# Kernel optimization log

Measured on AMD Instinct MI355X. Metric: run time of the kernel, lower is better.

The kernel has to match this reference:

```python
import jax, jax.numpy as jnp
import numpy as np

EPS = 1e-5
NUM_HEADS = 6


def _dwconv_bn(x5, W, g, b, m, v, stride):
    # x5: [B, C, H, W, D]; depthwise conv3d (groups=C), kernel 3, pad 1, then eval BatchNorm3d,
    # then rearrange 'b c h w d -> b (h w d) c'
    C = x5.shape[1]
    y = jax.lax.conv_general_dilated(
        x5, W, window_strides=(stride, stride, stride), padding=[(1, 1)] * 3,
        feature_group_count=C, dimension_numbers=('NCDHW', 'OIDHW', 'NCDHW'))
    inv = g / jnp.sqrt(v + EPS)
    y = y * inv[None, :, None, None, None] + (b - m * inv)[None, :, None, None, None]
    B, C2, H, Wd, D = y.shape
    return y.transpose(0, 2, 3, 4, 1).reshape(B, H * Wd * D, C2)


def setup_inputs() -> dict:
    key = jax.random.key(0)
    ks = jax.random.split(key, 24)
    B, T, C = 8, 4096, 384
    hh = ww = dd = 16
    s = 0.02
    inp = {
        'x': jax.random.normal(ks[0], (B, T, C), jnp.float32),
        'conv_q_w': jax.random.normal(ks[1], (C, 1, 3, 3, 3), jnp.float32) * 0.1,
        'conv_k_w': jax.random.normal(ks[2], (C, 1, 3, 3, 3), jnp.float32) * 0.1,
        'conv_v_w': jax.random.normal(ks[3], (C, 1, 3, 3, 3), jnp.float32) * 0.1,
        'bn_q_g': jax.random.uniform(ks[4], (C,), jnp.float32, 0.5, 1.5),
        'bn_q_b': jax.random.normal(ks[5], (C,), jnp.float32) * 0.1,
        'bn_q_m': jax.random.normal(ks[6], (C,), jnp.float32) * 0.1,
        'bn_q_v': jax.random.uniform(ks[7], (C,), jnp.float32, 0.5, 1.5),
        'bn_k_g': jax.random.uniform(ks[8], (C,), jnp.float32, 0.5, 1.5),
        'bn_k_b': jax.random.normal(ks[9], (C,), jnp.float32) * 0.1,
        'bn_k_m': jax.random.normal(ks[10], (C,), jnp.float32) * 0.1,
        'bn_k_v': jax.random.uniform(ks[11], (C,), jnp.float32, 0.5, 1.5),
        'bn_v_g': jax.random.uniform(ks[12], (C,), jnp.float32, 0.5, 1.5),
        'bn_v_b': jax.random.normal(ks[13], (C,), jnp.float32) * 0.1,
        'bn_v_m': jax.random.normal(ks[14], (C,), jnp.float32) * 0.1,
        'bn_v_v': jax.random.uniform(ks[15], (C,), jnp.float32, 0.5, 1.5),
        'wq': jax.random.normal(ks[16], (C, C), jnp.float32) * s,
        'wk': jax.random.normal(ks[17], (C, C), jnp.float32) * s,
        'wv': jax.random.normal(ks[18], (C, C), jnp.float32) * s,
        'proj_w': jax.random.normal(ks[19], (C, C), jnp.float32) * s,
        'proj_b': jax.random.normal(ks[20], (C,), jnp.float32) * s,
        'h': hh, 'w': ww, 'd': dd,
    }
    return inp


def reference(x, conv_q_w, conv_k_w, conv_v_w,
              bn_q_g, bn_q_b, bn_q_m, bn_q_v,
              bn_k_g, bn_k_b, bn_k_m, bn_k_v,
              bn_v_g, bn_v_b, bn_v_m, bn_v_v,
              wq, wk, wv, proj_w, proj_b, h, w, d):
    B, T, C = x.shape
    H = NUM_HEADS
    Dh = C // H
    scale = C ** (-0.5)  # dim_out ** -0.5
    x5 = x.reshape(B, h, w, d, C).transpose(0, 4, 1, 2, 3)  # b (h w d) c -> b c h w d
    q = _dwconv_bn(x5, conv_q_w, bn_q_g, bn_q_b, bn_q_m, bn_q_v, 1)   # [B, T, C]
    k = _dwconv_bn(x5, conv_k_w, bn_k_g, bn_k_b, bn_k_m, bn_k_v, 2)   # [B, Tkv, C]
    v = _dwconv_bn(x5, conv_v_w, bn_v_g, bn_v_b, bn_v_m, bn_v_v, 2)   # [B, Tkv, C]

    def to_heads(t, W):  # Linear (no bias) then 'b t (h d) -> b h t d'
        z = t @ W.T
        return z.reshape(B, -1, H, Dh).transpose(0, 2, 1, 3)

    q = to_heads(q, wq)
    k = to_heads(k, wk)
    v = to_heads(v, wv)
    attn = jax.nn.softmax(jnp.einsum('bhld,bhtd->bhlt', q, k) * scale, axis=-1)
    o = jnp.einsum('bhlt,bhtd->bhld', attn, v)
    o = o.transpose(0, 2, 1, 3).reshape(B, -1, C)  # b h t d -> b t (h d)
    return o @ proj_w.T + proj_b
```

## Files before the change

kernel.cpp:

```cpp
#include <hip/hip_runtime.h>
#include <hip/hip_bf16.h>
#include <stdint.h>


typedef _Float16 f16;
typedef _Float16 f16x8 __attribute__((ext_vector_type(8)));
typedef _Float16 f16x2 __attribute__((ext_vector_type(2)));
typedef float f32x4 __attribute__((ext_vector_type(4)));
typedef float f32x16 __attribute__((ext_vector_type(16)));
typedef uint32_t u32;
typedef uint32_t u32x4 __attribute__((ext_vector_type(4)));

#define NC 384
#define MFMA16(A_,B_,C_) __builtin_amdgcn_mfma_f32_16x16x32_f16((A_),(B_),(C_),0,0,0)
#define MFMA32(A_,B_,C_) __builtin_amdgcn_mfma_f32_32x32x16_f16((A_),(B_),(C_),0,0,0)

__device__ __forceinline__ void gll16(const void* g, void* l) {
  __builtin_amdgcn_global_load_lds(
      (__attribute__((address_space(1))) void*)g,
      (__attribute__((address_space(3))) void*)l, 16, 0, 0);
}

__device__ __forceinline__ u32 pkf16(float lo, float hi) {
  return __builtin_bit_cast(u32, __builtin_amdgcn_cvt_pkrtz(lo, hi));
}

__global__ __launch_bounds__(256) void cvt_w(
    const float* __restrict__ s0, const float* __restrict__ s1,
    const float* __restrict__ s2, const float* __restrict__ s3,
    f16* __restrict__ d0, f16* __restrict__ d1,
    f16* __restrict__ d2, f16* __restrict__ d3, int n, float scq)
{
  int i = blockIdx.x * 256 + threadIdx.x;
  if (i < n) {
    d0[i] = (f16)(s0[i] * scq);
    d1[i] = (f16)s1[i]; d2[i] = (f16)s2[i]; d3[i] = (f16)s3[i];
  }
}

__global__ __launch_bounds__(384) void cvt_wt(
    const float* __restrict__ wq, const float* __restrict__ wk, const float* __restrict__ wv,
    float* __restrict__ qT, float* __restrict__ kT, float* __restrict__ vT)
{
  const int c = threadIdx.x;
  const int t = blockIdx.x;
  qT[t * 384 + c] = wq[c * 27 + t];
  kT[t * 384 + c] = wk[c * 27 + t];
  vT[t * 384 + c] = wv[c * 27 + t];
}

__global__ __launch_bounds__(128) void conv_fused(
    const float* __restrict__ x,
    const float* __restrict__ wqT, const float* __restrict__ wkT, const float* __restrict__ wvT,
    const float* __restrict__ bqg, const float* __restrict__ bqb,
    const float* __restrict__ bqm, const float* __restrict__ bqv,
    const float* __restrict__ bkg, const float* __restrict__ bkb,
    const float* __restrict__ bkm, const float* __restrict__ bkv,
    const float* __restrict__ bvg, const float* __restrict__ bvb,
    const float* __restrict__ bvm, const float* __restrict__ bvv,
    f16* __restrict__ qout, f16* __restrict__ kout, f16* __restrict__ vout)
{
  const int tile = blockIdx.x / 3, cthird = blockIdx.x % 3;
  const int c = cthird * 128 + threadIdx.x;
  const int th = tile >> 3, tw = tile & 7;
  const int b = blockIdx.y;
  const int z0 = blockIdx.z * 8;
  const int h0 = th * 2, w0 = tw * 2;

  float wqr[27], wkr[27], wvr[27];
#pragma unroll
  for (int t = 0; t < 27; ++t) {
    wqr[t] = wqT[t * 384 + c];
    wkr[t] = wkT[t * 384 + c];
    wvr[t] = wvT[t * 384 + c];
  }
  float invq = bqg[c] * rsqrtf(bqv[c] + 1e-5f), betq = bqb[c] - bqm[c] * invq;
  float invk = bkg[c] * rsqrtf(bkv[c] + 1e-5f), betk = bkb[c] - bkm[c] * invk;
  float invv = bvg[c] * rsqrtf(bvv[c] + 1e-5f), betv = bvb[c] - bvm[c] * invv;

  bool hok[4], wok[4];
#pragma unroll
  for (int a = 0; a < 4; ++a) {
    hok[a] = (unsigned)(h0 - 1 + a) < 16u;
    wok[a] = (unsigned)(w0 - 1 + a) < 16u;
  }
  const float* xb = x + (size_t)b * 4096 * NC + c;

  float win[3][4][4];
  auto ldplane = [&](int s, int iz) {
    const bool zok = (unsigned)iz < 16u;
#pragma unroll
    for (int a = 0; a < 4; ++a)
#pragma unroll
      for (int e = 0; e < 4; ++e) {
        float v = 0.f;
        if (zok && hok[a] && wok[e])
          v = xb[(size_t)((h0 - 1 + a) * 256 + (w0 - 1 + e) * 16 + iz) * NC];
        win[s][a][e] = v;
      }
  };
  ldplane(2, z0 - 1);
  ldplane(0, z0);

#pragma unroll
  for (int zr = 0; zr < 8; ++zr) {
    const int z = z0 + zr;
    const int snew = (zr + 1) % 3;
    ldplane(snew, z + 1);
    float aq00 = 0.f, aq01 = 0.f, aq10 = 0.f, aq11 = 0.f;
    float ak = 0.f, av = 0.f;
#pragma unroll
    for (int p = 0; p < 3; ++p) {
      const int s = (zr - 1 + p + 3) % 3;
#pragma unroll
      for (int a = 0; a < 3; ++a)
#pragma unroll
        for (int e = 0; e < 3; ++e) {
          const float w00 = win[s][a][e],     w01 = win[s][a][e + 1];
          const float w10 = win[s][a + 1][e], w11 = win[s][a + 1][e + 1];
          const float cq = wqr[a * 9 + e * 3 + p];
          aq00 += w00 * cq; aq01 += w01 * cq;
          aq10 += w10 * cq; aq11 += w11 * cq;
          if ((zr & 1) == 0) {
            ak += w00 * wkr[a * 9 + e * 3 + p];
            av += w00 * wvr[a * 9 + e * 3 + p];
          }
        }
    }
    const size_t qb = (size_t)b * 4096;
    qout[(qb + (h0 + 0) * 256 + (w0 + 0) * 16 + z) * NC + c] = (f16)(aq00 * invq + betq);
    qout[(qb + (h0 + 0) * 256 + (w0 + 1) * 16 + z) * NC + c] = (f16)(aq01 * invq + betq);
    qout[(qb + (h0 + 1) * 256 + (w0 + 0) * 16 + z) * NC + c] = (f16)(aq10 * invq + betq);
    qout[(qb + (h0 + 1) * 256 + (w0 + 1) * 16 + z) * NC + c] = (f16)(aq11 * invq + betq);
    if ((zr & 1) == 0) {
      const size_t t = (size_t)b * 512 + (th * 8 + tw) * 8 + (z >> 1);
      kout[t * NC + c] = (f16)(ak * invk + betk);
      vout[t * NC + c] = (f16)(av * invv + betv);
    }
  }
}

template<int MODE>
__global__ __launch_bounds__(256) void gemm_bt(
    const f16* __restrict__ A, const f16* __restrict__ Bw,
    void* __restrict__ Cout, const float* __restrict__ bias)
{
  __shared__ f16 As[128 * 64];
  __shared__ f16 Bs[128 * 64];
  const int tid = threadIdx.x;
  const int w = tid >> 6, lane = tid & 63;
  const int g = lane >> 4, q = lane & 15;
  const int wr = w >> 1, wc = w & 1;
  const size_t brow = (size_t)blockIdx.y * 128;
  const int bcol = blockIdx.x * 128;
  const int srow = lane >> 3;
  const int sbb  = (lane & 7) ^ (srow & 7);
  f32x4 acc[4][4] = {};
  for (int kt = 0; kt < 6; ++kt) {
    const int k0 = kt * 64;
#pragma unroll
    for (int j = 0; j < 4; ++j) {
      const int s = w * 4 + j;
      gll16(A  + (brow + (size_t)(s * 8 + srow)) * NC + k0 + sbb * 8, (char*)As + s * 1024);
      gll16(Bw + (size_t)(bcol + s * 8 + srow) * NC + k0 + sbb * 8, (char*)Bs + s * 1024);
    }
    __syncthreads();
#pragma unroll
    for (int ks = 0; ks < 2; ++ks) {
      f16x8 af[4], bfr[4];
      const int bb = ((g + 4 * ks) ^ (q & 7)) * 16;
#pragma unroll
      for (int m = 0; m < 4; ++m) {
        af[m]  = *(const f16x8*)((const char*)As + (wr * 64 + m * 16 + q) * 128 + bb);
        bfr[m] = *(const f16x8*)((const char*)Bs + (wc * 64 + m * 16 + q) * 128 + bb);
      }
#pragma unroll
      for (int m = 0; m < 4; ++m)
#pragma unroll
        for (int n = 0; n < 4; ++n)
          acc[m][n] = MFMA16(af[m], bfr[n], acc[m][n]);
    }
    __syncthreads();
  }
  float bvals[4];
  if (MODE == 2) {
#pragma unroll
    for (int n = 0; n < 4; ++n) bvals[n] = bias[bcol + wc * 64 + n * 16 + q];
  }
#pragma unroll
  for (int m = 0; m < 4; ++m) {
#pragma unroll
    for (int n = 0; n < 4; ++n) {
#pragma unroll
      for (int r = 0; r < 4; ++r) {
        const size_t row = brow + wr * 64 + m * 16 + 4 * g + r;
        const int col = bcol + wc * 64 + n * 16 + q;
        const float v = acc[m][n][r];
        if (MODE == 0) {
          ((f16*)Cout)[row * NC + col] = (f16)v;
        } else if (MODE == 1) {
          const size_t bi = row >> 9, t = row & 511;
          ((f16*)Cout)[(bi * NC + col) * 512 + t] = (f16)v;
        } else {
          ((float*)Cout)[row * NC + col] = v + bvals[n];
        }
      }
    }
  }
}

__global__ __launch_bounds__(256) void attn(
    const f16* __restrict__ Qp, const f16* __restrict__ Kp,
    const f16* __restrict__ Vt, f16* __restrict__ O)
{
  __shared__ f16 Ks[2][64 * 64];
  __shared__ f16 Vs[2][64 * 64];
  const int tid = threadIdx.x;
  const int w = tid >> 6, lane = tid & 63;
  const int c = lane & 31, h = lane >> 5;
  const int qt = blockIdx.x, hh = blockIdx.y, b = blockIdx.z;
  const size_t qrow = (size_t)b * 4096 + qt * 128 + w * 32 + c;

  f16x8 qf[4];
#pragma unroll
  for (int ks = 0; ks < 4; ++ks)
    qf[ks] = *(const f16x8*)(Qp + qrow * NC + hh * 64 + ks * 16 + 8 * h);

  f32x16 oa0 = {}, oa1 = {};
  float l_run = 0.f;

  const int r0 = tid >> 3, k0b = tid & 7;
  const int r1 = (tid + 256) >> 3, k1b = tid & 7;
  const f16* ks0 = Kp + ((size_t)b * 512 + r0) * NC + hh * 64 + ((k0b ^ (r0 & 7)) * 8);
  const f16* ks1 = Kp + ((size_t)b * 512 + r1) * NC + hh * 64 + ((k1b ^ (r1 & 7)) * 8);
  const f16* vs0 = Vt + ((size_t)b * NC + hh * 64 + r0) * 512 + ((k0b ^ (r0 & 7)) * 8);
  const f16* vs1 = Vt + ((size_t)b * NC + hh * 64 + r1) * 512 + ((k1b ^ (r1 & 7)) * 8);
  gll16(ks0, (char*)&Ks[0][0] + tid * 16);
  gll16(ks1, (char*)&Ks[0][0] + (tid + 256) * 16);
  gll16(vs0, (char*)&Vs[0][0] + tid * 16);
  gll16(vs1, (char*)&Vs[0][0] + (tid + 256) * 16);

  int buf = 0;
  for (int ch = 0; ch < 8; ++ch) {
    __syncthreads();
    if (ch < 7) {
      gll16(ks0 + (size_t)(ch + 1) * 64 * NC, (char*)&Ks[buf ^ 1][0] + tid * 16);
      gll16(ks1 + (size_t)(ch + 1) * 64 * NC, (char*)&Ks[buf ^ 1][0] + (tid + 256) * 16);
      gll16(vs0 + (ch + 1) * 64, (char*)&Vs[buf ^ 1][0] + tid * 16);
      gll16(vs1 + (ch + 1) * 64, (char*)&Vs[buf ^ 1][0] + (tid + 256) * 16);
    }
    const char* kb = (const char*)&Ks[buf][0];
    const char* vb = (const char*)&Vs[buf][0];
#pragma unroll
    for (int half = 0; half < 2; ++half) {
      f32x16 st = {};
#pragma unroll
      for (int ks = 0; ks < 4; ++ks) {
        const int bo = ((2 * ks + h) ^ (c & 7)) * 16;
        const f16x8 kf = *(const f16x8*)(kb + (32 * half + c) * 128 + bo);
        st = MFMA32(kf, qf[ks], st);
      }
      u32 pk[8];
      float ps0 = 0.f, ps1 = 0.f;
#pragma unroll
      for (int t = 0; t < 8; ++t) {
        const float a0 = exp2f(st[2 * t]);
        const float a1 = exp2f(st[2 * t + 1]);
        ps0 += a0; ps1 += a1;
        pk[t] = pkf16(a0, a1);
      }
      l_run += ps0 + ps1;
#pragma unroll
      for (int ss = 0; ss < 2; ++ss) {
        const int s = half * 2 + ss, tb = ss * 4;
        const u32 xs = h ? pk[tb + 0] : pk[tb + 2];
        const u32 ys = h ? pk[tb + 1] : pk[tb + 3];
        const u32 rx = __shfl_xor(xs, 32);
        const u32 ry = __shfl_xor(ys, 32);
        u32x4 fi;
        fi[0] = h ? rx : pk[tb + 0];
        fi[1] = h ? ry : pk[tb + 1];
        fi[2] = h ? pk[tb + 2] : rx;
        fi[3] = h ? pk[tb + 3] : ry;
        const f16x8 pfrag = __builtin_bit_cast(f16x8, fi);
        const int bo = ((2 * s + h) ^ (c & 7)) * 16;
        const f16x8 v0 = *(const f16x8*)(vb + c * 128 + bo);
        const f16x8 v1 = *(const f16x8*)(vb + (32 + c) * 128 + bo);
        oa0 = MFMA32(v0, pfrag, oa0);
        oa1 = MFMA32(v1, pfrag, oa1);
      }
    }
    buf ^= 1;
  }
  const float ltot = l_run + __shfl_xor(l_run, 32);
  const float linv = 1.0f / ltot;
  f16* orow = O + qrow * NC + hh * 64;
#pragma unroll
  for (int dt = 0; dt < 2; ++dt) {
#pragma unroll
    for (int qd = 0; qd < 4; ++qd) {
      const float v0 = (dt ? oa1[4 * qd + 0] : oa0[4 * qd + 0]) * linv;
      const float v1 = (dt ? oa1[4 * qd + 1] : oa0[4 * qd + 1]) * linv;
      const float v2 = (dt ? oa1[4 * qd + 2] : oa0[4 * qd + 2]) * linv;
      const float v3 = (dt ? oa1[4 * qd + 3] : oa0[4 * qd + 3]) * linv;
      uint2 pr; pr.x = pkf16(v0, v1); pr.y = pkf16(v2, v3);
      *(uint2*)(orow + dt * 32 + 8 * qd + 4 * h) = pr;
    }
  }
}

extern "C" void kernel_launch(void* const* d_in, const int* in_sizes, int n_in,
                              void* d_out, int out_size, void* d_ws, size_t ws_size,
                              hipStream_t stream) {
  const float* x   = (const float*)d_in[0];
  const float* cqw = (const float*)d_in[1];
  const float* ckw = (const float*)d_in[2];
  const float* cvw = (const float*)d_in[3];
  const float* bqg = (const float*)d_in[4],  *bqb = (const float*)d_in[5];
  const float* bqm = (const float*)d_in[6],  *bqv = (const float*)d_in[7];
  const float* bkg = (const float*)d_in[8],  *bkb = (const float*)d_in[9];
  const float* bkm = (const float*)d_in[10], *bkv = (const float*)d_in[11];
  const float* bvg = (const float*)d_in[12], *bvb = (const float*)d_in[13];
  const float* bvm = (const float*)d_in[14], *bvv = (const float*)d_in[15];
  const float* wq = (const float*)d_in[16];
  const float* wk = (const float*)d_in[17];
  const float* wv = (const float*)d_in[18];
  const float* pw = (const float*)d_in[19];
  const float* pb = (const float*)d_in[20];

  f16* q_tok = (f16*)d_out;
  f16* Qp    = (f16*)((char*)d_out + 25165824);

  char* ws = (char*)d_ws;
  f16* wq_h  = (f16*)(ws + 0);
  f16* wk_h  = (f16*)(ws + 294912);
  f16* wv_h  = (f16*)(ws + 589824);
  f16* pw_h  = (f16*)(ws + 884736);
  f16* k_tok = (f16*)(ws + 1179648);
  f16* v_tok = (f16*)(ws + 4325376);
  f16* Kp    = (f16*)(ws + 7471104);
  f16* Vt    = (f16*)(ws + 10616832);
  f16* Oi    = (f16*)(ws + 13762560);
  float* wqT = (float*)(ws + 38928384);
  float* wkT = (float*)(ws + 38969856);
  float* wvT = (float*)(ws + 39011328);

  const float scq = 0.051031036307982884f * 1.4426950408889634f;
  cvt_w<<<dim3(576), dim3(256), 0, stream>>>(wq, wk, wv, pw, wq_h, wk_h, wv_h, pw_h,
                                             147456, scq);
  cvt_wt<<<dim3(27), dim3(384), 0, stream>>>(cqw, ckw, cvw, wqT, wkT, wvT);
  conv_fused<<<dim3(192, 8, 2), dim3(128), 0, stream>>>(
      x, wqT, wkT, wvT,
      bqg, bqb, bqm, bqv, bkg, bkb, bkm, bkv, bvg, bvb, bvm, bvv,
      q_tok, k_tok, v_tok);
  gemm_bt<0><<<dim3(3, 256), dim3(256), 0, stream>>>(q_tok, wq_h, Qp, nullptr);
  gemm_bt<0><<<dim3(3, 32),  dim3(256), 0, stream>>>(k_tok, wk_h, Kp, nullptr);
  gemm_bt<1><<<dim3(3, 32),  dim3(256), 0, stream>>>(v_tok, wv_h, Vt, nullptr);
  attn<<<dim3(32, 6, 8), dim3(256), 0, stream>>>(Qp, Kp, Vt, Oi);
  gemm_bt<2><<<dim3(3, 256), dim3(256), 0, stream>>>(Oi, pw_h, d_out, pb);
}
```

Baseline: 155.6 us.

## Split fused depthwise conv into separate Q and strided K/V kernels

Replaces the single conv kernel that computed Q, K and V together with two kernels. conv_q processes 4 z-slices per block, so it launches twice as many blocks, and holds only the Q weights. conv_kv keeps just a 3x3 window per plane for the strided K/V convs. The aim is to lower register pressure, raise occupancy and parallelism, and drop the divergent even-z K/V branch. The cost is one extra launch and a second read of x, plus extra halo loads from the shorter z runs.

```diff
diff --git a/kernel.cpp b/kernel.cpp
--- a/kernel.cpp
+++ b/kernel.cpp
@@ -5,7 +5,6 @@
 
 typedef _Float16 f16;
 typedef _Float16 f16x8 __attribute__((ext_vector_type(8)));
-typedef _Float16 f16x2 __attribute__((ext_vector_type(2)));
 typedef float f32x4 __attribute__((ext_vector_type(4)));
 typedef float f32x16 __attribute__((ext_vector_type(16)));
 typedef uint32_t u32;
@@ -49,16 +48,84 @@
   vT[t * 384 + c] = wv[c * 27 + t];
 }
 
-__global__ __launch_bounds__(128) void conv_fused(
-    const float* __restrict__ x,
-    const float* __restrict__ wqT, const float* __restrict__ wkT, const float* __restrict__ wvT,
+__global__ __launch_bounds__(128) void conv_q(
+    const float* __restrict__ x, const float* __restrict__ wqT,
     const float* __restrict__ bqg, const float* __restrict__ bqb,
     const float* __restrict__ bqm, const float* __restrict__ bqv,
+    f16* __restrict__ qout)
+{
+  const int tile = blockIdx.x / 3, cthird = blockIdx.x % 3;
+  const int c = cthird * 128 + threadIdx.x;
+  const int th = tile >> 3, tw = tile & 7;
+  const int b = blockIdx.y;
+  const int z0 = blockIdx.z * 4;
+  const int h0 = th * 2, w0 = tw * 2;
+
+  float wqr[27];
+#pragma unroll
+  for (int t = 0; t < 27; ++t) wqr[t] = wqT[t * 384 + c];
+  const float invq = bqg[c] * rsqrtf(bqv[c] + 1e-5f);
+  const float betq = bqb[c] - bqm[c] * invq;
+
+  bool hok[4], wok[4];
+#pragma unroll
+  for (int a = 0; a < 4; ++a) {
+    hok[a] = (unsigned)(h0 - 1 + a) < 16u;
+    wok[a] = (unsigned)(w0 - 1 + a) < 16u;
+  }
+  const float* xb = x + (size_t)b * 4096 * NC + c;
+
+  float win[3][4][4];
+  auto ldplane = [&](int s, int iz) {
+    const bool zok = (unsigned)iz < 16u;
+#pragma unroll
+    for (int a = 0; a < 4; ++a)
+#pragma unroll
+      for (int e = 0; e < 4; ++e) {
+        float v = 0.f;
+        if (zok && hok[a] && wok[e])
+          v = xb[(size_t)((h0 - 1 + a) * 256 + (w0 - 1 + e) * 16 + iz) * NC];
+        win[s][a][e] = v;
+      }
+  };
+  ldplane(0, z0 - 1);
+  ldplane(1, z0);
+
+#pragma unroll
+  for (int zr = 0; zr < 4; ++zr) {
+    const int z = z0 + zr;
+    ldplane((zr + 2) % 3, z + 1);
+    float aq00 = 0.f, aq01 = 0.f, aq10 = 0.f, aq11 = 0.f;
+#pragma unroll
+    for (int p = 0; p < 3; ++p) {
+      const int s = (zr + p) % 3;
+#pragma unroll
+      for (int a = 0; a < 3; ++a)
+#pragma unroll
+        for (int e = 0; e < 3; ++e) {
+          const float cq = wqr[a * 9 + e * 3 + p];
+          aq00 += win[s][a][e]         * cq;
+          aq01 += win[s][a][e + 1]     * cq;
+          aq10 += win[s][a + 1][e]     * cq;
+          aq11 += win[s][a + 1][e + 1] * cq;
+        }
+    }
+    const size_t qb = (size_t)b * 4096;
+    qout[(qb + (h0 + 0) * 256 + (w0 + 0) * 16 + z) * NC + c] = (f16)(aq00 * invq + betq);
+    qout[(qb + (h0 + 0) * 256 + (w0 + 1) * 16 + z) * NC + c] = (f16)(aq01 * invq + betq);
+    qout[(qb + (h0 + 1) * 256 + (w0 + 0) * 16 + z) * NC + c] = (f16)(aq10 * invq + betq);
+    qout[(qb + (h0 + 1) * 256 + (w0 + 1) * 16 + z) * NC + c] = (f16)(aq11 * invq + betq);
+  }
+}
+
+__global__ __launch_bounds__(128) void conv_kv(
+    const float* __restrict__ x,
+    const float* __restrict__ wkT, const float* __restrict__ wvT,
     const float* __restrict__ bkg, const float* __restrict__ bkb,
     const float* __restrict__ bkm, const float* __restrict__ bkv,
     const float* __restrict__ bvg, const float* __restrict__ bvb,
     const float* __restrict__ bvm, const float* __restrict__ bvv,
-    f16* __restrict__ qout, f16* __restrict__ kout, f16* __restrict__ vout)
+    f16* __restrict__ kout, f16* __restrict__ vout)
 {
   const int tile = blockIdx.x / 3, cthird = blockIdx.x % 3;
   const int c = cthird * 128 + threadIdx.x;
@@ -67,75 +134,58 @@
   const int z0 = blockIdx.z * 8;
   const int h0 = th * 2, w0 = tw * 2;
 
-  float wqr[27], wkr[27], wvr[27];
-#pragma unroll
-  for (int t = 0; t < 27; ++t) {
-    wqr[t] = wqT[t * 384 + c];
-    wkr[t] = wkT[t * 384 + c];
-    wvr[t] = wvT[t * 384 + c];
-  }
-  float invq = bqg[c] * rsqrtf(bqv[c] + 1e-5f), betq = bqb[c] - bqm[c] * invq;
-  float invk = bkg[c] * rsqrtf(bkv[c] + 1e-5f), betk = bkb[c] - bkm[c] * invk;
-  float invv = bvg[c] * rsqrtf(bvv[c] + 1e-5f), betv = bvb[c] - bvm[c] * invv;
-
-  bool hok[4], wok[4];
-#pragma unroll
-  for (int a = 0; a < 4; ++a) {
+  float wkr[27], wvr[27];
+#pragma unroll
+  for (int t = 0; t < 27; ++t) { wkr[t] = wkT[t * 384 + c]; wvr[t] = wvT[t * 384 + c]; }
+  const float invk = bkg[c] * rsqrtf(bkv[c] + 1e-5f), betk = bkb[c] - bkm[c] * invk;
+  const float invv = bvg[c] * rsqrtf(bvv[c] + 1e-5f), betv = bvb[c] - bvm[c] * invv;
+
+  bool hok[3], wok[3];
+#pragma unroll
+  for (int a = 0; a < 3; ++a) {
     hok[a] = (unsigned)(h0 - 1 + a) < 16u;
     wok[a] = (unsigned)(w0 - 1 + a) < 16u;
   }
   const float* xb = x + (size_t)b * 4096 * NC + c;
 
-  float win[3][4][4];
-  auto ldplane = [&](int s, int iz) {
+  float wn[3][3][3];
+  auto ldplane3 = [&](int s, int iz) {
     const bool zok = (unsigned)iz < 16u;
 #pragma unroll
-    for (int a = 0; a < 4; ++a)
-#pragma unroll
-      for (int e = 0; e < 4; ++e) {
+    for (int a = 0; a < 3; ++a)
+#pragma unroll
+      for (int e = 0; e < 3; ++e) {
         float v = 0.f;
         if (zok && hok[a] && wok[e])
           v = xb[(size_t)((h0 - 1 + a) * 256 + (w0 - 1 + e) * 16 + iz) * NC];
-        win[s][a][e] = v;
+        wn[s][a][e] = v;
       }
   };
-  ldplane(2, z0 - 1);
-  ldplane(0, z0);
-
-#pragma unroll
-  for (int zr = 0; zr < 8; ++zr) {
-    const int z = z0 + zr;
-    const int snew = (zr + 1) % 3;
-    ldplane(snew, z + 1);
-    float aq00 = 0.f, aq01 = 0.f, aq10 = 0.f, aq11 = 0.f;
+  ldplane3(0, z0 - 1);
+  ldplane3(1, z0);
+  ldplane3(2, z0 + 1);
+#pragma unroll
+  for (int i = 0; i < 4; ++i) {
     float ak = 0.f, av = 0.f;
 #pragma unroll
     for (int p = 0; p < 3; ++p) {
-      const int s = (zr - 1 + p + 3) % 3;
+      const int s = (2 * i + p) % 3;
 #pragma unroll
       for (int a = 0; a < 3; ++a)
 #pragma unroll
         for (int e = 0; e < 3; ++e) {
-          const float w00 = win[s][a][e],     w01 = win[s][a][e + 1];
-          const float w10 = win[s][a + 1][e], w11 = win[s][a + 1][e + 1];
-          const float cq = wqr[a * 9 + e * 3 + p];
-          aq00 += w00 * cq; aq01 += w01 * cq;
-          aq10 += w10 * cq; aq11 += w11 * cq;
-          if ((zr & 1) == 0) {
-            ak += w00 * wkr[a * 9 + e * 3 + p];
-            av += w00 * wvr[a * 9 + e * 3 + p];
-          }
+          const float wv_ = wn[s][a][e];
+          ak += wv_ * wkr[a * 9 + e * 3 + p];
+          av += wv_ * wvr[a * 9 + e * 3 + p];
         }
     }
-    const size_t qb = (size_t)b * 4096;
-    qout[(qb + (h0 + 0) * 256 + (w0 + 0) * 16 + z) * NC + c] = (f16)(aq00 * invq + betq);
-    qout[(qb + (h0 + 0) * 256 + (w0 + 1) * 16 + z) * NC + c] = (f16)(aq01 * invq + betq);
-    qout[(qb + (h0 + 1) * 256 + (w0 + 0) * 16 + z) * NC + c] = (f16)(aq10 * invq + betq);
-    qout[(qb + (h0 + 1) * 256 + (w0 + 1) * 16 + z) * NC + c] = (f16)(aq11 * invq + betq);
-    if ((zr & 1) == 0) {
-      const size_t t = (size_t)b * 512 + (th * 8 + tw) * 8 + (z >> 1);
-      kout[t * NC + c] = (f16)(ak * invk + betk);
-      vout[t * NC + c] = (f16)(av * invv + betv);
+    const int zc = z0 + 2 * i;
+    const size_t t = (size_t)b * 512 + (th * 8 + tw) * 8 + (zc >> 1);
+    kout[t * NC + c] = (f16)(ak * invk + betk);
+    vout[t * NC + c] = (f16)(av * invv + betv);
+    if (i < 3) {
+      ldplane3((2 * i + 3) % 3, zc + 2);
+      ldplane3((2 * i + 4) % 3, zc + 3);
     }
   }
 }
@@ -349,10 +399,10 @@
   cvt_w<<<dim3(576), dim3(256), 0, stream>>>(wq, wk, wv, pw, wq_h, wk_h, wv_h, pw_h,
                                              147456, scq);
   cvt_wt<<<dim3(27), dim3(384), 0, stream>>>(cqw, ckw, cvw, wqT, wkT, wvT);
-  conv_fused<<<dim3(192, 8, 2), dim3(128), 0, stream>>>(
-      x, wqT, wkT, wvT,
-      bqg, bqb, bqm, bqv, bkg, bkb, bkm, bkv, bvg, bvb, bvm, bvv,
-      q_tok, k_tok, v_tok);
+  conv_q<<<dim3(192, 8, 4), dim3(128), 0, stream>>>(
+      x, wqT, bqg, bqb, bqm, bqv, q_tok);
+  conv_kv<<<dim3(192, 8, 2), dim3(128), 0, stream>>>(
+      x, wkT, wvT, bkg, bkb, bkm, bkv, bvg, bvb, bvm, bvv, k_tok, v_tok);
   gemm_bt<0><<<dim3(3, 256), dim3(256), 0, stream>>>(q_tok, wq_h, Qp, nullptr);
   gemm_bt<0><<<dim3(3, 32),  dim3(256), 0, stream>>>(k_tok, wk_h, Kp, nullptr);
   gemm_bt<1><<<dim3(3, 32),  dim3(256), 0, stream>>>(v_tok, wv_h, Vt, nullptr);
```

New measurement: 192.2 us. 1.23x slower.
